# Kernel optimization log

Measured on AMD Instinct MI355X. Metric: run time of the kernel, lower is better.

## Reference

```python
import jax, jax.numpy as jnp
import numpy as np

NUM_HEADS = 10
LN_EPS = 1e-5


def setup_inputs() -> dict:
    key = jax.random.key(0)
    ks = jax.random.split(key, 6)
    N, D = 4096, 640  # in_dim == out_dim required by residual add
    x = jax.random.normal(ks[0], (N, D), dtype=jnp.float32)
    s = 1.0 / np.sqrt(D)
    Wq = jax.random.normal(ks[1], (D, D), dtype=jnp.float32) * s  # torch Linear weight [out,in]
    Wk = jax.random.normal(ks[2], (D, D), dtype=jnp.float32) * s
    Wv = jax.random.normal(ks[3], (D, D), dtype=jnp.float32) * s
    gamma = jnp.ones((D,), dtype=jnp.float32)
    beta = jnp.zeros((D,), dtype=jnp.float32)
    return {"x": x, "Wq": Wq, "Wk": Wk, "Wv": Wv, "gamma": gamma, "beta": beta}


def reference(x, Wq, Wk, Wv, gamma, beta):
    N, D = x.shape
    dk = D // NUM_HEADS
    Q = x @ Wq.T  # [N, D]
    K = x @ Wk.T
    V = x @ Wv.T
    # Faithful to source: raw reshapes (NOT transposes)
    Qh = Q.reshape(NUM_HEADS, N, dk)
    Kh = K.reshape(NUM_HEADS, N, dk).reshape(NUM_HEADS, dk, N)  # torch.reshape, not .mT
    Vh = V.reshape(NUM_HEADS, N, dk)
    # Faithful quirk: scale by sqrt(K.shape[2]) == sqrt(N)
    scale = np.float32(np.sqrt(N))
    wghts = jax.nn.softmax((Qh @ Kh) / scale, axis=-1)  # [H, N, N]
    values = wghts @ Vh  # [H, N, dk]
    values = values.reshape(N, NUM_HEADS * dk)  # raw reshape merge
    values = values + x  # residual
    # LayerNorm(out_dim), biased variance, eps=1e-5
    mean = jnp.mean(values, axis=-1, keepdims=True)
    var = jnp.mean(jnp.square(values - mean), axis=-1, keepdims=True)
    out = (values - mean) * jax.lax.rsqrt(var + LN_EPS) * gamma + beta
    return out
```

## Files before the change

### kernel.cpp

```cpp
#include <hip/hip_runtime.h>
#if __has_include(<hip/hip_fp8.h>)
#include <hip/hip_fp8.h>
#endif


typedef __bf16 bf16x8 __attribute__((ext_vector_type(8)));
typedef __bf16 bf16x4 __attribute__((ext_vector_type(4)));
typedef float  f32x4  __attribute__((ext_vector_type(4)));
typedef unsigned short u16x4 __attribute__((ext_vector_type(4)));
typedef unsigned int   u32x4 __attribute__((ext_vector_type(4)));
typedef u32x4          u32x4a __attribute__((may_alias));
typedef long           la64  __attribute__((may_alias));
typedef unsigned int   ua32  __attribute__((may_alias));

#define N_TOK   4096
#define D_MODEL 640
#define DK      64
#define HSLAB   (N_TOK * DK)
#define SQS 0.15014030f

#if __has_builtin(__builtin_amdgcn_exp2f)
#define EXP2(x) __builtin_amdgcn_exp2f(x)
#else
#define EXP2(x) exp2f(x)
#endif

__device__ __forceinline__ void stage16(const void* g, void* lds_uniform) {
    __builtin_amdgcn_global_load_lds(
        (const __attribute__((address_space(1))) unsigned int*)g,
        (__attribute__((address_space(3))) unsigned int*)lds_uniform, 16, 0, 0);
}

__device__ __forceinline__ u16x4 cvt4(f32x4 v) {
    return __builtin_bit_cast(u16x4, __builtin_convertvector(v, bf16x4));
}

__device__ __forceinline__ unsigned int pk_fp8(f32x4 v) {
#if __has_builtin(__builtin_amdgcn_cvt_pk_fp8_f32)
    int r = 0;
    r = __builtin_amdgcn_cvt_pk_fp8_f32(v[0], v[1], r, false);
    r = __builtin_amdgcn_cvt_pk_fp8_f32(v[2], v[3], r, true);
    return (unsigned int)r;
#else
    union { unsigned char b[4]; unsigned int u; } x;
    x.b[0] = __hip_fp8_e4m3(v[0]).__x;
    x.b[1] = __hip_fp8_e4m3(v[1]).__x;
    x.b[2] = __hip_fp8_e4m3(v[2]).__x;
    x.b[3] = __hip_fp8_e4m3(v[3]).__x;
    return x.u;
#endif
}

__global__ __launch_bounds__(256) void cvt_all(const float* __restrict__ x,
                                               const float* __restrict__ w0,
                                               const float* __restrict__ w1,
                                               const float* __restrict__ w2,
                                               unsigned short* __restrict__ xb,
                                               unsigned short* __restrict__ d0,
                                               unsigned short* __restrict__ d1,
                                               unsigned short* __restrict__ d2,
                                               f32x4* __restrict__ ltot4) {
    int i = blockIdx.x * 256 + threadIdx.x;
    if (i >= 962560) { ltot4[i - 962560] = (f32x4){0.f, 0.f, 0.f, 0.f}; return; }
    const float* s; unsigned short* d; int off; float scl = 1.0f;
    if (i < 655360) { s = x; d = xb; off = i; }
    else {
        int j = i - 655360;
        int w = j / 102400; off = j - w * 102400;
        s = (w == 0) ? w0 : (w == 1) ? w1 : w2;
        d = (w == 0) ? d0 : (w == 1) ? d1 : d2;
        if (w < 2) scl = SQS;
    }
    f32x4 v = ((const f32x4*)s)[off];
    v[0] *= scl; v[1] *= scl; v[2] *= scl; v[3] *= scl;
    ((u16x4*)d)[off] = cvt4(v);
}

__global__ __launch_bounds__(256, 2) void gemm_qkv(
    const unsigned short* __restrict__ xb,
    const unsigned short* __restrict__ wq,
    const unsigned short* __restrict__ wk,
    const unsigned short* __restrict__ wv,
    unsigned char*  __restrict__ Qf8o,
    unsigned short* __restrict__ Ko,
    unsigned short* __restrict__ Vo) {
    const int b = blockIdx.x;
    const int g = b & 31;
    const int r = b >> 5;
    const int mode = r / 5;
    const int m0 = g * 128;
    const int n0 = (r % 5) * 128;
    const unsigned short* W = (mode == 0) ? wq : (mode == 1) ? wk : wv;
    unsigned short*       C = (mode == 1) ? Ko : Vo;

    __shared__ unsigned short As[8192];
    __shared__ unsigned short Bs[8192];

    const int tid  = threadIdx.x;
    const int lane = tid & 63;
    const int wave = tid >> 6;
    const int quad = lane >> 4, l16 = lane & 15;
    const int wm = (wave >> 1) * 64, wn = (wave & 1) * 64;
    const int swz = l16 & 7;

    f32x4 acc[4][4] = {};

    int prow[4], pcol[4], lbase[4];
    for (int j = 0; j < 4; j++) {
        int p = j * 256 + tid;
        prow[j] = p >> 3;
        pcol[j] = ((p & 7) ^ (prow[j] & 7)) * 8;
        lbase[j] = (j * 256 + wave * 64) * 8;
    }

    for (int kt = 0; kt < D_MODEL; kt += 64) {
        __syncthreads();
        for (int j = 0; j < 4; j++) {
            stage16(&xb[(size_t)(m0 + prow[j]) * D_MODEL + kt + pcol[j]], As + lbase[j]);
            stage16(&W [(size_t)(n0 + prow[j]) * D_MODEL + kt + pcol[j]], Bs + lbase[j]);
        }
        __syncthreads();

        for (int s = 0; s < 2; s++) {
            bf16x8 af[4], bfr[4];
            for (int mi = 0; mi < 4; mi++) {
                int row = wm + mi * 16 + l16;
                af[mi] = *(const bf16x8*)&As[row * 64 + (((s << 2) + quad) ^ swz) * 8];
            }
            for (int ni = 0; ni < 4; ni++) {
                int row = wn + ni * 16 + l16;
                bfr[ni] = *(const bf16x8*)&Bs[row * 64 + (((s << 2) + quad) ^ swz) * 8];
            }
            for (int mi = 0; mi < 4; mi++)
                for (int ni = 0; ni < 4; ni++)
                    acc[mi][ni] = __builtin_amdgcn_mfma_f32_16x16x32_bf16(af[mi], bfr[ni], acc[mi][ni], 0, 0, 0);
        }
    }

    if (mode == 0) {
        for (int mi = 0; mi < 4; mi++)
            for (int ni = 0; ni < 4; ni++) {
                unsigned int p = pk_fp8(acc[mi][ni]);
                for (int r2 = 0; r2 < 4; r2++) {
                    int row = m0 + wm + mi * 16 + quad * 4 + r2;
                    int col = n0 + wn + ni * 16 + l16;
                    Qf8o[(size_t)row * D_MODEL + col] = (unsigned char)(p >> (r2 * 8));
                }
            }
    } else {
        for (int mi = 0; mi < 4; mi++)
            for (int ni = 0; ni < 4; ni++) {
                u16x4 cv = cvt4(acc[mi][ni]);
                for (int r2 = 0; r2 < 4; r2++) {
                    int row = m0 + wm + mi * 16 + quad * 4 + r2;
                    int col = n0 + wn + ni * 16 + l16;
                    C[(size_t)row * D_MODEL + col] = cv[r2];
                }
            }
    }
}

__global__ __launch_bounds__(256) void transpose_kv(
    const unsigned short* __restrict__ Kn, unsigned char* __restrict__ Kp8,
    const unsigned short* __restrict__ Vn, unsigned char* __restrict__ Vp8) {
    const int z = blockIdx.z;
    const int t = threadIdx.x;

    __shared__ unsigned short T[64][66];
    const unsigned short* src; unsigned char* dst;
    int R, Cc, r0, c0;
    if (z < 10) { src = Kn; dst = Kp8; R = 64;   Cc = 4096; r0 = 0; c0 = blockIdx.x * 64; }
    else        { src = Vn; dst = Vp8; R = 4096; Cc = 64;   r0 = blockIdx.x * 64; c0 = 0; }
    const size_t hb = (size_t)(z % 10) * HSLAB;
    const int rr = t >> 3, c8 = (t & 7) * 8;

    for (int hf = 0; hf < 2; hf++) {
        int r = rr + hf * 32;
        bf16x8 v = *(const bf16x8*)&src[hb + (size_t)(r0 + r) * Cc + c0 + c8];
        for (int j = 0; j < 8; j++) T[r][c8 + j] = ((unsigned short*)&v)[j];
    }
    __syncthreads();
    const bf16x8 zz = {};
    for (int hf = 0; hf < 2; hf++) {
        int r = rr + hf * 32;
        *(bf16x8*)&((unsigned short*)src)[hb + (size_t)(r0 + r) * Cc + c0 + c8] = zz;
    }
    for (int hf = 0; hf < 2; hf++) {
        int oc = rr + hf * 32;
        f32x4 lo, hi;
        for (int j = 0; j < 4; j++) {
            lo[j] = __builtin_bit_cast(float, (unsigned int)T[c8 + j][oc] << 16);
            hi[j] = __builtin_bit_cast(float, (unsigned int)T[c8 + 4 + j][oc] << 16);
        }
        uint2 ov; ov.x = pk_fp8(lo); ov.y = pk_fp8(hi);
        size_t dcol = (z < 10) ? ((size_t)(c0 + oc) * 64 + r0 + c8)
                               : ((size_t)oc * 4096 + r0 + c8);
        *(uint2*)&dst[hb + dcol] = ov;
    }
}

__global__ __launch_bounds__(256, 4) void attn(
    const unsigned char* __restrict__ Qf8,
    const unsigned char* __restrict__ Kp8,
    const unsigned char* __restrict__ Vp8,
    float* __restrict__ vals,
    float* __restrict__ l_tot) {
    const int h  = blockIdx.x >> 5;
    const int qt = blockIdx.x & 31;
    const int ntile = (blockIdx.y == 2) ? 10 : 11;
    const int tile0 = blockIdx.y * 11;
    const int lane = threadIdx.x & 63;
    const int wave = threadIdx.x >> 6;
    const int quad = lane >> 4, l16 = lane & 15;
    const size_t hoff = (size_t)h * HSLAB;

    __shared__ unsigned char sm[32768];
    unsigned char* const Kb = sm;
    unsigned char* const Vt = sm + 8192;
    unsigned char* const Pw = sm + 16384 + wave * 4096;

    const int qbase = qt * 128 + wave * 32;
    long qd[2][2];
    for (int g = 0; g < 2; g++) {
        const unsigned char* qp = Qf8 + hoff + (size_t)(qbase + g * 16 + l16) * 64 + quad * 8;
        qd[g][0] = *(const la64*)(qp);
        qd[g][1] = *(const la64*)(qp + 32);
    }

    f32x4 o[2][4] = {};
    f32x4 ol[2] = {};
    const long ONES8 = 0x3838383838383838L;

    const int cA = wave * 64 + lane, cB = cA + 256;
    const int kKeyA = ((cA >> 5) << 3) + (cA & 7), kCiA = (cA >> 3) & 3;
    const int kKeyB = ((cB >> 5) << 3) + (cB & 7), kCiB = (cB >> 3) & 3;
    const int vDkA  = ((cA >> 6) << 3) + (cA & 7), vCvA = (cA >> 3) & 7;
    const int vDkB  = ((cB >> 6) << 3) + (cB & 7), vCvB = (cB >> 3) & 7;

    const int kfb = (l16 >> 3) * 512 + (quad >> 1) * 128 + (l16 & 7) * 16 + (quad & 1) * 8;
    const int vfb = (l16 >> 3) * 1024 + (quad >> 1) * 128 + (l16 & 7) * 16 + (quad & 1) * 8;

    {
        const int keyb = tile0 << 7;
        stage16(Kp8 + hoff + (size_t)(keyb + kKeyA) * 64 + kCiA * 16, Kb + wave * 1024);
        stage16(Kp8 + hoff + (size_t)(keyb + kKeyB) * 64 + kCiB * 16, Kb + 4096 + wave * 1024);
    }

    for (int t = 0; t < ntile; t++) {
        const int keyb = (tile0 + t) << 7;

        __syncthreads();

        u32x4 kr0, kr1;
        const bool pf_k = (t + 1 < ntile);
        if (pf_k) {
            const int keyn = (tile0 + t + 1) << 7;
            kr0 = *(const u32x4a*)(Kp8 + hoff + (size_t)(keyn + kKeyA) * 64 + kCiA * 16);
            kr1 = *(const u32x4a*)(Kp8 + hoff + (size_t)(keyn + kKeyB) * 64 + kCiB * 16);
        }
        stage16(Vp8 + hoff + (size_t)vDkA * N_TOK + keyb + vCvA * 16, Vt + wave * 1024);
        stage16(Vp8 + hoff + (size_t)vDkB * N_TOK + keyb + vCvB * 16, Vt + 4096 + wave * 1024);

        for (int ni = 0; ni < 8; ni++) {
            const unsigned char* kp = Kb + ni * 1024 + kfb;
            long a0 = *(const la64*)(kp);
            long a1 = *(const la64*)(kp + 256);
            for (int g = 0; g < 2; g++) {
                f32x4 s = {};
                __builtin_amdgcn_s_setprio(1);
                s = __builtin_amdgcn_mfma_f32_16x16x32_fp8_fp8(a0, qd[g][0], s, 0, 0, 0);
                s = __builtin_amdgcn_mfma_f32_16x16x32_fp8_fp8(a1, qd[g][1], s, 0, 0, 0);
                __builtin_amdgcn_s_setprio(0);
                f32x4 pv;
                for (int r = 0; r < 4; r++) pv[r] = EXP2(s[r]);
                const int pu = ni * 2 + (quad >> 1);
                *(ua32*)(Pw + pu * 256 +
                         (((g * 16 + l16) + ((pu & 3) << 3)) & 31) * 8 +
                         (quad & 1) * 4) = pk_fp8(pv);
            }
        }

        __syncthreads();

        if (pf_k) {
            *(u32x4a*)(Kb + (size_t)cA * 16) = kr0;
            *(u32x4a*)(Kb + (size_t)cB * 16) = kr1;
        }

        for (int ks = 0; ks < 4; ks++) {
            long vf[4];
            for (int nd = 0; nd < 4; nd++)
                vf[nd] = *(const la64*)(Vt + nd * 2048 + ks * 256 + vfb);
            for (int g = 0; g < 2; g++) {
                long pf = *(const la64*)(Pw + (ks * 4 + quad) * 256 +
                                         (((g * 16 + l16) + (quad << 3)) & 31) * 8);
                __builtin_amdgcn_s_setprio(1);
                ol[g] = __builtin_amdgcn_mfma_f32_16x16x32_fp8_fp8(pf, ONES8, ol[g], 0, 0, 0);
                for (int nd = 0; nd < 4; nd++)
                    o[g][nd] = __builtin_amdgcn_mfma_f32_16x16x32_fp8_fp8(pf, vf[nd], o[g][nd], 0, 0, 0);
                __builtin_amdgcn_s_setprio(0);
            }
        }
    }

    if (l16 == 0)
        for (int g = 0; g < 2; g++)
            for (int r = 0; r < 4; r++)
                atomicAdd(&l_tot[(h << 12) + qbase + g * 16 + quad * 4 + r], ol[g][r]);

    for (int g = 0; g < 2; g++)
        for (int nd = 0; nd < 4; nd++)
            for (int r = 0; r < 4; r++) {
                int q = qbase + g * 16 + quad * 4 + r;
                atomicAdd(&vals[hoff + (size_t)q * DK + nd * 16 + l16], o[g][nd][r]);
            }
}

__global__ __launch_bounds__(256) void ln_kernel(
    const float* __restrict__ vals, const float* __restrict__ l_tot,
    const float* __restrict__ x,
    const float* __restrict__ gamma, const float* __restrict__ beta,
    float* __restrict__ out) {
    const int wave = threadIdx.x >> 6, lane = threadIdx.x & 63;
    const int row  = blockIdx.x * 4 + wave;
    const float* v  = vals + (size_t)row * D_MODEL;
    const float* xr = x    + (size_t)row * D_MODEL;

    float t[10];
    float s = 0.f;
    for (int i = 0; i < 10; i++) {
        float linv = 1.0f / l_tot[row * 10 + i];
        t[i] = v[lane + i * 64] * linv + xr[lane + i * 64];
        s += t[i];
    }
    for (int off = 32; off; off >>= 1) s += __shfl_xor(s, off, 64);
    float mean = s * (1.0f / 640.0f);
    float s2 = 0.f;
    for (int i = 0; i < 10; i++) { float d = t[i] - mean; s2 += d * d; }
    for (int off = 32; off; off >>= 1) s2 += __shfl_xor(s2, off, 64);
    float inv = rsqrtf(s2 * (1.0f / 640.0f) + 1e-5f);

    float* orow = out + (size_t)row * D_MODEL;
    for (int i = 0; i < 10; i++) {
        int c = lane + i * 64;
        orow[c] = (t[i] - mean) * inv * gamma[c] + beta[c];
    }
}

extern "C" void kernel_launch(void* const* d_in, const int* in_sizes, int n_in,
                              void* d_out, int out_size, void* d_ws, size_t ws_size,
                              hipStream_t stream) {
    const float* x     = (const float*)d_in[0];
    const float* Wq    = (const float*)d_in[1];
    const float* Wk    = (const float*)d_in[2];
    const float* Wv    = (const float*)d_in[3];
    const float* gamma = (const float*)d_in[4];
    const float* beta  = (const float*)d_in[5];
    float* out = (float*)d_out;

    char* ws = (char*)d_ws;
    unsigned short* xb  = (unsigned short*)(ws);
    unsigned short* wqb = (unsigned short*)(ws + 5242880);
    unsigned short* wkb = (unsigned short*)(ws + 6062080);
    unsigned short* wvb = (unsigned short*)(ws + 6881280);
    unsigned char*  Qf8 = (unsigned char*)(ws + 7700480);
    unsigned char*  Kp8 = (unsigned char*)(ws + 12943360);
    unsigned char*  Vp8 = (unsigned char*)(ws + 18186240);
    unsigned short* Kn  = (unsigned short*)(ws + 23429120);
    unsigned short* Vn  = (unsigned short*)(ws + 28672000);
    float*          vals  = (float*)(ws + 23429120);
    float*          l_tot = (float*)(ws + 33914880);

    cvt_all<<<3800, 256, 0, stream>>>(x, Wq, Wk, Wv, xb, wqb, wkb, wvb,
                                      (f32x4*)l_tot);

    gemm_qkv<<<480, 256, 0, stream>>>(xb, wqb, wkb, wvb, Qf8, Kn, Vn);

    transpose_kv<<<dim3(64, 1, 20), 256, 0, stream>>>(Kn, Kp8, Vn, Vp8);

    attn<<<dim3(320, 3), 256, 0, stream>>>(Qf8, Kp8, Vp8, vals, l_tot);
    ln_kernel<<<1024, 256, 0, stream>>>(vals, l_tot, x, gamma, beta, out);
}
```

Measured before the change: 151.9 us.

## Double-buffer K/V tiles via async LDS loads and compute row sums in fp32

Replaces the single K/V LDS buffers with double buffers filled by asynchronous global-to-LDS loads one tile ahead. Vmcnt waits and raw s_barrier replace the register-staged K prefetch and the two __syncthreads per tile. The softmax denominator is now summed from the fp32 exp values with lane shuffles instead of an extra ones-vector fp8 MFMA per step. This removes MFMA work and hides load latency, but LDS use grows from 32KB to 48KB, which can lower occupancy. The denominator now uses unquantized exps while the PV product still uses fp8-rounded P.

```diff
diff --git a/kernel.cpp b/kernel.cpp
--- a/kernel.cpp
+++ b/kernel.cpp
@@ -9,7 +9,6 @@
 typedef float  f32x4  __attribute__((ext_vector_type(4)));
 typedef unsigned short u16x4 __attribute__((ext_vector_type(4)));
 typedef unsigned int   u32x4 __attribute__((ext_vector_type(4)));
-typedef u32x4          u32x4a __attribute__((may_alias));
 typedef long           la64  __attribute__((may_alias));
 typedef unsigned int   ua32  __attribute__((may_alias));
 
@@ -214,10 +213,10 @@
     const int quad = lane >> 4, l16 = lane & 15;
     const size_t hoff = (size_t)h * HSLAB;
 
-    __shared__ unsigned char sm[32768];
+    __shared__ unsigned char sm[49152];
     unsigned char* const Kb = sm;
-    unsigned char* const Vt = sm + 8192;
-    unsigned char* const Pw = sm + 16384 + wave * 4096;
+    unsigned char* const Vb = sm + 16384;
+    unsigned char* const Pw = sm + 32768 + wave * 4096;
 
     const int qbase = qt * 128 + wave * 32;
     long qd[2][2];
@@ -228,8 +227,7 @@
     }
 
     f32x4 o[2][4] = {};
-    f32x4 ol[2] = {};
-    const long ONES8 = 0x3838383838383838L;
+    float lsum[2] = {0.f, 0.f};
 
     const int cA = wave * 64 + lane, cB = cA + 256;
     const int kKeyA = ((cA >> 5) << 3) + (cA & 7), kCiA = (cA >> 3) & 3;
@@ -240,29 +238,35 @@
     const int kfb = (l16 >> 3) * 512 + (quad >> 1) * 128 + (l16 & 7) * 16 + (quad & 1) * 8;
     const int vfb = (l16 >> 3) * 1024 + (quad >> 1) * 128 + (l16 & 7) * 16 + (quad & 1) * 8;
 
-    {
-        const int keyb = tile0 << 7;
-        stage16(Kp8 + hoff + (size_t)(keyb + kKeyA) * 64 + kCiA * 16, Kb + wave * 1024);
-        stage16(Kp8 + hoff + (size_t)(keyb + kKeyB) * 64 + kCiB * 16, Kb + 4096 + wave * 1024);
-    }
+#define STAGE_K(t_) do { const int kb_ = (tile0 + (t_)) << 7;                         \
+        unsigned char* const d_ = Kb + (((t_) & 1) << 13);                            \
+        stage16(Kp8 + hoff + (size_t)(kb_ + kKeyA) * 64 + kCiA * 16, d_ + wave * 1024);        \
+        stage16(Kp8 + hoff + (size_t)(kb_ + kKeyB) * 64 + kCiB * 16, d_ + 4096 + wave * 1024); \
+    } while (0)
+#define STAGE_V(t_) do { const int kb_ = (tile0 + (t_)) << 7;                         \
+        unsigned char* const d_ = Vb + (((t_) & 1) << 13);                            \
+        stage16(Vp8 + hoff + (size_t)vDkA * N_TOK + kb_ + vCvA * 16, d_ + wave * 1024);        \
+        stage16(Vp8 + hoff + (size_t)vDkB * N_TOK + kb_ + vCvB * 16, d_ + 4096 + wave * 1024); \
+    } while (0)
+
+    STAGE_K(0); STAGE_V(0);
 
     for (int t = 0; t < ntile; t++) {
-        const int keyb = (tile0 + t) << 7;
-
-        __syncthreads();
-
-        u32x4 kr0, kr1;
-        const bool pf_k = (t + 1 < ntile);
-        if (pf_k) {
-            const int keyn = (tile0 + t + 1) << 7;
-            kr0 = *(const u32x4a*)(Kp8 + hoff + (size_t)(keyn + kKeyA) * 64 + kCiA * 16);
-            kr1 = *(const u32x4a*)(Kp8 + hoff + (size_t)(keyn + kKeyB) * 64 + kCiB * 16);
-        }
-        stage16(Vp8 + hoff + (size_t)vDkA * N_TOK + keyb + vCvA * 16, Vt + wave * 1024);
-        stage16(Vp8 + hoff + (size_t)vDkB * N_TOK + keyb + vCvB * 16, Vt + 4096 + wave * 1024);
+        __builtin_amdgcn_s_barrier();
+        if (t + 1 < ntile) {
+            STAGE_K(t + 1); STAGE_V(t + 1);
+            asm volatile("s_waitcnt vmcnt(4)" ::: "memory");
+        } else {
+            asm volatile("s_waitcnt vmcnt(0)" ::: "memory");
+        }
+        __builtin_amdgcn_s_barrier();
+        __builtin_amdgcn_sched_barrier(0);
+
+        const unsigned char* const Kcur = Kb + ((t & 1) << 13);
+        const unsigned char* const Vcur = Vb + ((t & 1) << 13);
 
         for (int ni = 0; ni < 8; ni++) {
-            const unsigned char* kp = Kb + ni * 1024 + kfb;
+            const unsigned char* kp = Kcur + ni * 1024 + kfb;
             long a0 = *(const la64*)(kp);
             long a1 = *(const la64*)(kp + 256);
             for (int g = 0; g < 2; g++) {
@@ -273,6 +277,7 @@
                 __builtin_amdgcn_s_setprio(0);
                 f32x4 pv;
                 for (int r = 0; r < 4; r++) pv[r] = EXP2(s[r]);
+                lsum[g] += (pv[0] + pv[1]) + (pv[2] + pv[3]);
                 const int pu = ni * 2 + (quad >> 1);
                 *(ua32*)(Pw + pu * 256 +
                          (((g * 16 + l16) + ((pu & 3) << 3)) & 31) * 8 +
@@ -280,33 +285,30 @@
             }
         }
 
-        __syncthreads();
-
-        if (pf_k) {
-            *(u32x4a*)(Kb + (size_t)cA * 16) = kr0;
-            *(u32x4a*)(Kb + (size_t)cB * 16) = kr1;
-        }
-
         for (int ks = 0; ks < 4; ks++) {
             long vf[4];
             for (int nd = 0; nd < 4; nd++)
-                vf[nd] = *(const la64*)(Vt + nd * 2048 + ks * 256 + vfb);
+                vf[nd] = *(const la64*)(Vcur + nd * 2048 + ks * 256 + vfb);
             for (int g = 0; g < 2; g++) {
                 long pf = *(const la64*)(Pw + (ks * 4 + quad) * 256 +
                                          (((g * 16 + l16) + (quad << 3)) & 31) * 8);
                 __builtin_amdgcn_s_setprio(1);
-                ol[g] = __builtin_amdgcn_mfma_f32_16x16x32_fp8_fp8(pf, ONES8, ol[g], 0, 0, 0);
                 for (int nd = 0; nd < 4; nd++)
                     o[g][nd] = __builtin_amdgcn_mfma_f32_16x16x32_fp8_fp8(pf, vf[nd], o[g][nd], 0, 0, 0);
                 __builtin_amdgcn_s_setprio(0);
             }
         }
     }
-
-    if (l16 == 0)
-        for (int g = 0; g < 2; g++)
-            for (int r = 0; r < 4; r++)
-                atomicAdd(&l_tot[(h << 12) + qbase + g * 16 + quad * 4 + r], ol[g][r]);
+#undef STAGE_K
+#undef STAGE_V
+
+    for (int g = 0; g < 2; g++) {
+        float ls = lsum[g];
+        ls += __shfl_xor(ls, 16, 64);
+        ls += __shfl_xor(ls, 32, 64);
+        if (quad == 0)
+            atomicAdd(&l_tot[(h << 12) + qbase + g * 16 + l16], ls);
+    }
 
     for (int g = 0; g < 2; g++)
         for (int nd = 0; nd < 4; nd++)
```

Result: slower. 161.6 us (+6.3%).

## Load K and V MFMA fragments directly from global memory, drop LDS staging

Applied to the files above, without the earlier changes.

Removes the shared-memory staging of K (register prefetch plus LDS write) and V (global_load_lds) in the attention kernel. Each lane now reads its K and V fp8 fragments straight from global memory, which eliminates both per-tile __syncthreads and cuts LDS use from 32KB to 16KB, allowing higher occupancy. In exchange, each of the four waves redundantly fetches the same K/V tiles through the cache with small 8-byte loads and no software prefetch, so global and L2 traffic and load latency rise.

```diff
diff --git a/kernel.cpp b/kernel.cpp
--- a/kernel.cpp
+++ b/kernel.cpp
@@ -9,7 +9,6 @@
 typedef float  f32x4  __attribute__((ext_vector_type(4)));
 typedef unsigned short u16x4 __attribute__((ext_vector_type(4)));
 typedef unsigned int   u32x4 __attribute__((ext_vector_type(4)));
-typedef u32x4          u32x4a __attribute__((may_alias));
 typedef long           la64  __attribute__((may_alias));
 typedef unsigned int   ua32  __attribute__((may_alias));
 
@@ -214,10 +213,8 @@
     const int quad = lane >> 4, l16 = lane & 15;
     const size_t hoff = (size_t)h * HSLAB;
 
-    __shared__ unsigned char sm[32768];
-    unsigned char* const Kb = sm;
-    unsigned char* const Vt = sm + 8192;
-    unsigned char* const Pw = sm + 16384 + wave * 4096;
+    __shared__ unsigned char sm[16384];
+    unsigned char* const Pw = sm + wave * 4096;
 
     const int qbase = qt * 128 + wave * 32;
     long qd[2][2];
@@ -231,40 +228,17 @@
     f32x4 ol[2] = {};
     const long ONES8 = 0x3838383838383838L;
 
-    const int cA = wave * 64 + lane, cB = cA + 256;
-    const int kKeyA = ((cA >> 5) << 3) + (cA & 7), kCiA = (cA >> 3) & 3;
-    const int kKeyB = ((cB >> 5) << 3) + (cB & 7), kCiB = (cB >> 3) & 3;
-    const int vDkA  = ((cA >> 6) << 3) + (cA & 7), vCvA = (cA >> 3) & 7;
-    const int vDkB  = ((cB >> 6) << 3) + (cB & 7), vCvB = (cB >> 3) & 7;
-
-    const int kfb = (l16 >> 3) * 512 + (quad >> 1) * 128 + (l16 & 7) * 16 + (quad & 1) * 8;
-    const int vfb = (l16 >> 3) * 1024 + (quad >> 1) * 128 + (l16 & 7) * 16 + (quad & 1) * 8;
-
-    {
-        const int keyb = tile0 << 7;
-        stage16(Kp8 + hoff + (size_t)(keyb + kKeyA) * 64 + kCiA * 16, Kb + wave * 1024);
-        stage16(Kp8 + hoff + (size_t)(keyb + kKeyB) * 64 + kCiB * 16, Kb + 4096 + wave * 1024);
-    }
+    const unsigned char* Kfrag = Kp8 + hoff + ((size_t)(tile0 << 7) + (size_t)l16) * 64 + quad * 8;
+    const unsigned char* Vfrag = Vp8 + hoff + (size_t)l16 * N_TOK + (tile0 << 7) + quad * 8;
 
     for (int t = 0; t < ntile; t++) {
-        const int keyb = (tile0 + t) << 7;
-
-        __syncthreads();
-
-        u32x4 kr0, kr1;
-        const bool pf_k = (t + 1 < ntile);
-        if (pf_k) {
-            const int keyn = (tile0 + t + 1) << 7;
-            kr0 = *(const u32x4a*)(Kp8 + hoff + (size_t)(keyn + kKeyA) * 64 + kCiA * 16);
-            kr1 = *(const u32x4a*)(Kp8 + hoff + (size_t)(keyn + kKeyB) * 64 + kCiB * 16);
-        }
-        stage16(Vp8 + hoff + (size_t)vDkA * N_TOK + keyb + vCvA * 16, Vt + wave * 1024);
-        stage16(Vp8 + hoff + (size_t)vDkB * N_TOK + keyb + vCvB * 16, Vt + 4096 + wave * 1024);
+        const unsigned char* const Kt = Kfrag + (size_t)t * 8192;
+        const unsigned char* const Vt = Vfrag + t * 128;
 
         for (int ni = 0; ni < 8; ni++) {
-            const unsigned char* kp = Kb + ni * 1024 + kfb;
+            const unsigned char* kp = Kt + ni * 1024;
             long a0 = *(const la64*)(kp);
-            long a1 = *(const la64*)(kp + 256);
+            long a1 = *(const la64*)(kp + 32);
             for (int g = 0; g < 2; g++) {
                 f32x4 s = {};
                 __builtin_amdgcn_s_setprio(1);
@@ -280,17 +254,10 @@
             }
         }
 
-        __syncthreads();
-
-        if (pf_k) {
-            *(u32x4a*)(Kb + (size_t)cA * 16) = kr0;
-            *(u32x4a*)(Kb + (size_t)cB * 16) = kr1;
-        }
-
         for (int ks = 0; ks < 4; ks++) {
             long vf[4];
             for (int nd = 0; nd < 4; nd++)
-                vf[nd] = *(const la64*)(Vt + nd * 2048 + ks * 256 + vfb);
+                vf[nd] = *(const la64*)(Vt + (size_t)nd * (16 * N_TOK) + ks * 32);
             for (int g = 0; g < 2; g++) {
                 long pf = *(const la64*)(Pw + (ks * 4 + quad) * 256 +
                                          (((g * 16 + l16) + (quad << 3)) & 31) * 8);
```

Measured after the change: 226.4 us. 1.49x slower.
